# Performance work log

Hardware: AMD Instinct MI355X
Metric: run time of the kernel (lower is better)

The kernel has to match this reference:

```python
import jax, jax.numpy as jnp
import numpy as np

N = 50000


def gcn_conv(x, W, b, src, dst, deg_inv_sqrt):
    # h = x @ W, then symmetric-normalized aggregation with self-loops
    h = x @ W  # [N, out]
    norm = deg_inv_sqrt[src] * deg_inv_sqrt[dst]  # [E]
    agg = jax.ops.segment_sum(h[src] * norm[:, None], dst, num_segments=N)
    # self-loop contribution: norm_ii = deg_inv_sqrt[i]^2
    agg = agg + h * (deg_inv_sqrt * deg_inv_sqrt)[:, None]
    return agg + b


def setup_inputs() -> dict:
    key = jax.random.key(0)
    ks = jax.random.split(key, 8)
    F_in, H, C = 128, 128, 64
    x = jax.random.normal(ks[0], (N, F_in), dtype=jnp.float32)
    edge_index = jax.random.randint(ks[1], (2, 800000), 0, N, dtype=jnp.int64)
    s = 1.0 / np.sqrt(F_in)
    W1 = jax.random.uniform(ks[2], (F_in, H), jnp.float32, -s, s)
    b1 = jnp.zeros((H,), jnp.float32)
    W2 = jax.random.uniform(ks[3], (H, H), jnp.float32, -s, s)
    b2 = jnp.zeros((H,), jnp.float32)
    W3 = jax.random.uniform(ks[4], (H, C), jnp.float32, -s, s)
    b3 = jnp.zeros((C,), jnp.float32)
    return {"x": x, "edge_index": edge_index, "W1": W1, "b1": b1,
            "W2": W2, "b2": b2, "W3": W3, "b3": b3}


def reference(x, edge_index, W1, b1, W2, b2, W3, b3):
    src, dst = edge_index[0], edge_index[1]
    # degree with self-loops (edge weight 1): deg[i] = in-degree + 1
    deg = jnp.zeros((N,), x.dtype).at[dst].add(1.0) + 1.0
    dinv = jax.lax.rsqrt(deg)
    h = gcn_conv(x, W1, b1, src, dst, dinv)
    h = jax.nn.relu(h)  # dropout p=0 / eval -> identity
    h = gcn_conv(h, W2, b2, src, dst, dinv)
    h = jax.nn.relu(h)
    h = gcn_conv(h, W3, b3, src, dst, dinv)
    return jax.nn.log_softmax(h, axis=-1)
```

## Files before the change

### kernel.cpp

```cpp
#include <hip/hip_runtime.h>
#include <math.h>

typedef short short8 __attribute__((ext_vector_type(8)));
typedef float floatx4 __attribute__((ext_vector_type(4)));

#define CHUNK_SHIFT 13
#define NCHUNK 8

__device__ __forceinline__ float4 ld4(const float* p) { return *reinterpret_cast<const float4*>(p); }
__device__ __forceinline__ void st4(float* p, float4 v) { *reinterpret_cast<float4*>(p) = v; }

__device__ __forceinline__ float bf2f(unsigned int u) { return __uint_as_float(u << 16); }
__device__ __forceinline__ unsigned int f2bf1(float f) {
    unsigned int x = __float_as_uint(f);
    return (x + 0x7fffu + ((x >> 16) & 1u)) >> 16;
}
__device__ __forceinline__ unsigned int f2bf2(float lo, float hi) {
    return f2bf1(lo) | (f2bf1(hi) << 16);
}
__device__ __forceinline__ void unpack8(uint4 v, float* f) {
    f[0] = bf2f(v.x & 0xffffu); f[1] = bf2f(v.x >> 16);
    f[2] = bf2f(v.y & 0xffffu); f[3] = bf2f(v.y >> 16);
    f[4] = bf2f(v.z & 0xffffu); f[5] = bf2f(v.z >> 16);
    f[6] = bf2f(v.w & 0xffffu); f[7] = bf2f(v.w >> 16);
}

__device__ __forceinline__ int sum8(const int* __restrict__ p) {
    uint4 a = *reinterpret_cast<const uint4*>(p);
    uint4 b = *reinterpret_cast<const uint4*>(p + 4);
    return (int)(a.x + a.y + a.z + a.w + b.x + b.y + b.z + b.w);
}

__global__ __launch_bounds__(256) void k_count_prep(const int* __restrict__ src, const int* __restrict__ dst,
                                                    int* __restrict__ deg2, int* __restrict__ rank, int E, int nbE,
                                                    const float* __restrict__ W1, const float* __restrict__ W2,
                                                    const float* __restrict__ W3, unsigned short* __restrict__ Wt1,
                                                    unsigned short* __restrict__ Wt2, unsigned short* __restrict__ Wt3) {
    if ((int)blockIdx.x < nbE) {
        int e = blockIdx.x * 256 + threadIdx.x;
        if (e < E) {
            int c = src[e] >> CHUNK_SHIFT;
            rank[e] = atomicAdd(&deg2[dst[e] * NCHUNK + c], 1);
        }
    } else {
        int t = (blockIdx.x - nbE) * 256 + threadIdx.x;
        if (t < 16384) {
            int k = t & 127, n = t >> 7;
            Wt1[n * 128 + k] = (unsigned short)f2bf1(W1[(size_t)k * 128 + n]);
        } else if (t < 32768) {
            int u = t - 16384;
            int k = u & 127, n = u >> 7;
            Wt2[n * 128 + k] = (unsigned short)f2bf1(W2[(size_t)k * 128 + n]);
        } else if (t < 40960) {
            int u = t - 32768;
            int k = u & 127, n = u >> 7;
            Wt3[n * 128 + k] = (unsigned short)f2bf1(W3[(size_t)k * 64 + n]);
        }
    }
}

__global__ __launch_bounds__(256) void k_dinv_reduce(const int* __restrict__ deg2, float* __restrict__ dinv,
                                                     int* __restrict__ bsum, int n, int nbN) {
    __shared__ int s[256];
    int t = threadIdx.x;
    if ((int)blockIdx.x < nbN) {
        int i = blockIdx.x * 256 + t;
        if (i < n) {
            int d = sum8(deg2 + (size_t)i * NCHUNK);
            dinv[i] = 1.0f / sqrtf((float)d + 1.0f);
        }
        return;
    }
    int b = (int)blockIdx.x - nbN;
    int i = b * 256 + t;
    s[t] = (i < n) ? sum8(deg2 + (size_t)i * NCHUNK) : 0;
    __syncthreads();
    for (int off = 128; off > 0; off >>= 1) {
        if (t < off) s[t] += s[t + off];
        __syncthreads();
    }
    if (t == 0) bsum[b] = s[0];
}

__global__ __launch_bounds__(256) void k_scansmall_gemm1(const int* __restrict__ bsum, int* __restrict__ boff, int nb,
                                                         const float* __restrict__ X, const unsigned short* __restrict__ Wt,
                                                         const float* __restrict__ dinv,
                                                         unsigned short* __restrict__ O, int nrows) {
    constexpr int LDR = 136;
    __shared__ __align__(16) unsigned char smem[(64 * LDR + 128 * LDR) * 2];

    const int tid = threadIdx.x;
    if (blockIdx.x == 0) {
        int* s = (int*)smem;
        int v = (tid < nb) ? bsum[tid] : 0;
        s[tid] = v;
        __syncthreads();
        for (int off = 1; off < 256; off <<= 1) {
            int x = (tid >= off) ? s[tid - off] : 0;
            __syncthreads();
            s[tid] += x;
            __syncthreads();
        }
        if (tid < nb) boff[tid] = s[tid] - v;
        return;
    }

    unsigned short* sX = (unsigned short*)smem;
    unsigned short* sB = sX + 64 * LDR;
    const int row0 = ((int)blockIdx.x - 1) * 64;

#pragma unroll
    for (int i = 0; i < 4; ++i) {
        int idx = tid + i * 256;
        int r = idx >> 4, c8 = idx & 15;
        int grow = row0 + r;
        uint4 v = make_uint4(0, 0, 0, 0);
        if (grow < nrows) {
            float4 a = ld4(X + (size_t)grow * 128 + c8 * 8);
            float4 b = ld4(X + (size_t)grow * 128 + c8 * 8 + 4);
            v = make_uint4(f2bf2(a.x, a.y), f2bf2(a.z, a.w), f2bf2(b.x, b.y), f2bf2(b.z, b.w));
        }
        *reinterpret_cast<uint4*>(&sX[r * LDR + c8 * 8]) = v;
    }
#pragma unroll
    for (int i = 0; i < 8; ++i) {
        int idx = tid + i * 256;
        int nn = idx >> 4, c8 = idx & 15;
        *reinterpret_cast<uint4*>(&sB[nn * LDR + c8 * 8]) =
            *reinterpret_cast<const uint4*>(Wt + (size_t)nn * 128 + c8 * 8);
    }
    __syncthreads();

    const int lane = tid & 63;
    const int wave = tid >> 6;
    const int l15  = lane & 15;
    const int quad = lane >> 4;

    floatx4 acc[8];
#pragma unroll
    for (int j = 0; j < 8; ++j) acc[j] = (floatx4){0.f, 0.f, 0.f, 0.f};

    const unsigned short* xbase = &sX[(wave * 16 + l15) * LDR + quad * 8];
#pragma unroll
    for (int kk = 0; kk < 4; ++kk) {
        short8 xb = *reinterpret_cast<const short8*>(xbase + kk * 32);
#pragma unroll
        for (int j = 0; j < 8; ++j) {
            short8 wa = *reinterpret_cast<const short8*>(&sB[(j * 16 + l15) * LDR + quad * 8 + kk * 32]);
            acc[j] = __builtin_amdgcn_mfma_f32_16x16x32_bf16(wa, xb, acc[j], 0, 0, 0);
        }
    }

    int xrow = row0 + wave * 16 + l15;
    if (xrow < nrows) {
        float di = dinv[xrow];
#pragma unroll
        for (int j = 0; j < 8; ++j) {
            uint2 o = make_uint2(f2bf2(acc[j][0] * di, acc[j][1] * di), f2bf2(acc[j][2] * di, acc[j][3] * di));
            *reinterpret_cast<uint2*>(O + (size_t)xrow * 128 + j * 16 + quad * 4) = o;
        }
    }
}

__global__ __launch_bounds__(256) void k_scan_final(const int* __restrict__ deg2, const int* __restrict__ boff,
                                                    int* __restrict__ row_off, int* __restrict__ starts2,
                                                    int n) {
    __shared__ int s[256];
    int t = threadIdx.x;
    int i = blockIdx.x * 256 + t;
    uint4 d0 = make_uint4(0, 0, 0, 0), d1 = make_uint4(0, 0, 0, 0);
    int tot = 0;
    if (i < n) {
        d0 = *reinterpret_cast<const uint4*>(deg2 + (size_t)i * NCHUNK);
        d1 = *reinterpret_cast<const uint4*>(deg2 + (size_t)i * NCHUNK + 4);
        tot = (int)(d0.x + d0.y + d0.z + d0.w + d1.x + d1.y + d1.z + d1.w);
    }
    s[t] = tot;
    __syncthreads();
    for (int off = 1; off < 256; off <<= 1) {
        int x = (t >= off) ? s[t - off] : 0;
        __syncthreads();
        s[t] += x;
        __syncthreads();
    }
    int incl = s[t] + boff[blockIdx.x];
    if (i < n) {
        int r = incl - tot;
        row_off[i] = r;
        uint4 o0, o1;
        o0.x = r; r += d0.x;
        o0.y = r; r += d0.y;
        o0.z = r; r += d0.z;
        o0.w = r; r += d0.w;
        o1.x = r; r += d1.x;
        o1.y = r; r += d1.y;
        o1.z = r; r += d1.z;
        o1.w = r;
        *reinterpret_cast<uint4*>(starts2 + (size_t)i * NCHUNK) = o0;
        *reinterpret_cast<uint4*>(starts2 + (size_t)i * NCHUNK + 4) = o1;
        if (i == n - 1) row_off[n] = incl;
    }
}

__global__ __launch_bounds__(256) void k_fill(const int* __restrict__ src, const int* __restrict__ dst,
                                              const int* __restrict__ rank, const int* __restrict__ starts2,
                                              int* __restrict__ csrc, int E) {
    int e = blockIdx.x * 256 + threadIdx.x;
    if (e < E) {
        int s = src[e];
        int c = s >> CHUNK_SHIFT;
        csrc[starts2[dst[e] * NCHUNK + c] + rank[e]] = s;
    }
}

template <int NC>
__global__ __launch_bounds__(256) void k_gemm_mfma(const unsigned short* __restrict__ X,
                                                   const unsigned short* __restrict__ Wt,
                                                   const float* __restrict__ dinv,
                                                   unsigned short* __restrict__ O, int nrows) {
    constexpr int LDR = 136;
    __shared__ unsigned short sX[64 * LDR];
    __shared__ unsigned short sB[NC * LDR];

    const int tid  = threadIdx.x;
    const int row0 = blockIdx.x * 64;

#pragma unroll
    for (int i = 0; i < 4; ++i) {
        int idx = tid + i * 256;
        int r = idx >> 4, c8 = idx & 15;
        int grow = row0 + r;
        uint4 v = make_uint4(0, 0, 0, 0);
        if (grow < nrows) v = *reinterpret_cast<const uint4*>(X + (size_t)grow * 128 + c8 * 8);
        *reinterpret_cast<uint4*>(&sX[r * LDR + c8 * 8]) = v;
    }
#pragma unroll
    for (int i = 0; i < NC / 16; ++i) {
        int idx = tid + i * 256;
        int n = idx >> 4, c8 = idx & 15;
        *reinterpret_cast<uint4*>(&sB[n * LDR + c8 * 8]) =
            *reinterpret_cast<const uint4*>(Wt + (size_t)n * 128 + c8 * 8);
    }
    __syncthreads();

    const int lane = tid & 63;
    const int wave = tid >> 6;
    const int l15  = lane & 15;
    const int quad = lane >> 4;

    floatx4 acc[NC / 16];
#pragma unroll
    for (int j = 0; j < NC / 16; ++j) acc[j] = (floatx4){0.f, 0.f, 0.f, 0.f};

    const unsigned short* xbase = &sX[(wave * 16 + l15) * LDR + quad * 8];
#pragma unroll
    for (int kk = 0; kk < 4; ++kk) {
        short8 xb = *reinterpret_cast<const short8*>(xbase + kk * 32);
#pragma unroll
        for (int j = 0; j < NC / 16; ++j) {
            short8 wa = *reinterpret_cast<const short8*>(&sB[(j * 16 + l15) * LDR + quad * 8 + kk * 32]);
            acc[j] = __builtin_amdgcn_mfma_f32_16x16x32_bf16(wa, xb, acc[j], 0, 0, 0);
        }
    }

    int xrow = row0 + wave * 16 + l15;
    if (xrow < nrows) {
        float di = dinv[xrow];
#pragma unroll
        for (int j = 0; j < NC / 16; ++j) {
            uint2 o = make_uint2(f2bf2(acc[j][0] * di, acc[j][1] * di), f2bf2(acc[j][2] * di, acc[j][3] * di));
            *reinterpret_cast<uint2*>(O + (size_t)xrow * NC + j * 16 + quad * 4) = o;
        }
    }
}

__global__ __launch_bounds__(256) void k_agg_relu(const unsigned short* __restrict__ H, const int* __restrict__ roff,
                                                  const int* __restrict__ csrc, const float* __restrict__ dinv,
                                                  const float* __restrict__ bias, unsigned short* __restrict__ O, int n) {
    int t      = blockIdx.x * 256 + threadIdx.x;
    int node   = t >> 5;
    int lane32 = t & 31;
    int half   = lane32 >> 4;
    int f8     = (lane32 & 15) * 8;
    if (node >= n) return;

    float a[8];
    if (half == 0) {
        uint4 hv = *reinterpret_cast<const uint4*>(H + (size_t)node * 128 + f8);
        unpack8(hv, a);
    } else {
#pragma unroll
        for (int i = 0; i < 8; ++i) a[i] = 0.0f;
    }

    int e0 = roff[node];
    int e1 = roff[node + 1];
    int mid = e0 + ((e1 - e0) >> 1);
    int e  = half ? mid : e0;
    int ee = half ? e1 : mid;

    for (; e + 3 < ee; e += 4) {
        int s[4];
        uint4 v[4];
#pragma unroll
        for (int u = 0; u < 4; ++u) s[u] = csrc[e + u];
#pragma unroll
        for (int u = 0; u < 4; ++u) v[u] = *reinterpret_cast<const uint4*>(H + (size_t)s[u] * 128 + f8);
#pragma unroll
        for (int u = 0; u < 4; ++u) {
            float g2[8];
            unpack8(v[u], g2);
#pragma unroll
            for (int i = 0; i < 8; ++i) a[i] += g2[i];
        }
    }
    for (; e < ee; ++e) {
        uint4 v0 = *reinterpret_cast<const uint4*>(H + (size_t)csrc[e] * 128 + f8);
        float g0[8];
        unpack8(v0, g0);
#pragma unroll
        for (int i = 0; i < 8; ++i) a[i] += g0[i];
    }

#pragma unroll
    for (int i = 0; i < 8; ++i) a[i] += __shfl_xor(a[i], 16);

    if (half == 0) {
        float di = dinv[node];
        float4 b0 = ld4(bias + f8);
        float4 b1 = ld4(bias + f8 + 4);
        float bb[8] = {b0.x, b0.y, b0.z, b0.w, b1.x, b1.y, b1.z, b1.w};
#pragma unroll
        for (int i = 0; i < 8; ++i) a[i] = fmaxf(a[i] * di + bb[i], 0.0f);

        uint4 ov = make_uint4(f2bf2(a[0], a[1]), f2bf2(a[2], a[3]), f2bf2(a[4], a[5]), f2bf2(a[6], a[7]));
        *reinterpret_cast<uint4*>(O + (size_t)node * 128 + f8) = ov;
    }
}

__global__ __launch_bounds__(256) void k_agg_softmax(const unsigned short* __restrict__ H, const int* __restrict__ roff,
                                                     const int* __restrict__ csrc, const float* __restrict__ dinv,
                                                     const float* __restrict__ bias, float* __restrict__ O, int n) {
    int t      = blockIdx.x * 256 + threadIdx.x;
    int node   = t >> 4;
    int lane16 = t & 15;
    int half   = lane16 >> 3;
    int f8     = (lane16 & 7) * 8;
    if (node >= n) return;

    float a[8];
    if (half == 0) {
        uint4 hv = *reinterpret_cast<const uint4*>(H + (size_t)node * 64 + f8);
        unpack8(hv, a);
    } else {
#pragma unroll
        for (int i = 0; i < 8; ++i) a[i] = 0.0f;
    }

    int e0 = roff[node];
    int e1 = roff[node + 1];
    int mid = e0 + ((e1 - e0) >> 1);
    int e  = half ? mid : e0;
    int ee = half ? e1 : mid;

    for (; e + 3 < ee; e += 4) {
        int s[4];
        uint4 v[4];
#pragma unroll
        for (int u = 0; u < 4; ++u) s[u] = csrc[e + u];
#pragma unroll
        for (int u = 0; u < 4; ++u) v[u] = *reinterpret_cast<const uint4*>(H + (size_t)s[u] * 64 + f8);
#pragma unroll
        for (int u = 0; u < 4; ++u) {
            float gg[8];
            unpack8(v[u], gg);
#pragma unroll
            for (int i = 0; i < 8; ++i) a[i] += gg[i];
        }
    }
    for (; e < ee; ++e) {
        uint4 v0 = *reinterpret_cast<const uint4*>(H + (size_t)csrc[e] * 64 + f8);
        float g0[8];
        unpack8(v0, g0);
#pragma unroll
        for (int i = 0; i < 8; ++i) a[i] += g0[i];
    }

#pragma unroll
    for (int i = 0; i < 8; ++i) a[i] += __shfl_xor(a[i], 8);

    if (half == 0) {
        float di = dinv[node];
        float4 b0 = ld4(bias + f8);
        float4 b1 = ld4(bias + f8 + 4);
        float bb[8] = {b0.x, b0.y, b0.z, b0.w, b1.x, b1.y, b1.z, b1.w};
        float v[8];
#pragma unroll
        for (int i = 0; i < 8; ++i) v[i] = a[i] * di + bb[i];

        float m = v[0];
#pragma unroll
        for (int i = 1; i < 8; ++i) m = fmaxf(m, v[i]);
        m = fmaxf(m, __shfl_xor(m, 1));
        m = fmaxf(m, __shfl_xor(m, 2));
        m = fmaxf(m, __shfl_xor(m, 4));

        float ssum = 0.0f;
#pragma unroll
        for (int i = 0; i < 8; ++i) ssum += expf(v[i] - m);
        ssum += __shfl_xor(ssum, 1);
        ssum += __shfl_xor(ssum, 2);
        ssum += __shfl_xor(ssum, 4);
        float ls = logf(ssum);

        float* op = O + (size_t)node * 64 + f8;
        st4(op, make_float4(v[0] - m - ls, v[1] - m - ls, v[2] - m - ls, v[3] - m - ls));
        st4(op + 4, make_float4(v[4] - m - ls, v[5] - m - ls, v[6] - m - ls, v[7] - m - ls));
    }
}

extern "C" void kernel_launch(void* const* d_in, const int* in_sizes, int n_in,
                              void* d_out, int out_size, void* d_ws, size_t ws_size,
                              hipStream_t stream) {
    const float* x  = (const float*)d_in[0];
    const int*   ei = (const int*)d_in[1];
    const float* W1 = (const float*)d_in[2];
    const float* b1 = (const float*)d_in[3];
    const float* W2 = (const float*)d_in[4];
    const float* b2 = (const float*)d_in[5];
    const float* W3 = (const float*)d_in[6];
    const float* b3 = (const float*)d_in[7];
    float* out = (float*)d_out;

    const int N = in_sizes[0] / 128;
    const int E = in_sizes[1] / 2;
    const int* src = ei;
    const int* dst = ei + E;

    char* ws = (char*)d_ws;
    size_t off = 0;
    auto alloc = [&](size_t bytes) -> char* {
        char* p = ws + off;
        off = (off + bytes + 255) & ~(size_t)255;
        return p;
    };
    int nb  = (N + 255) / 256;
    int nbE = (E + 255) / 256;
    int blocks64 = (N + 63) / 64;

    int*   deg2    = (int*)alloc((size_t)N * NCHUNK * 4);
    int*   row_off = (int*)alloc(((size_t)N + 1) * 4);
    int*   starts2 = (int*)alloc((size_t)N * NCHUNK * 4);
    float* dinv    = (float*)alloc((size_t)N * 4);
    int*   bsum    = (int*)alloc((size_t)nb * 4);
    int*   boff    = (int*)alloc((size_t)nb * 4);
    int*   rank    = (int*)alloc((size_t)E * 4);
    int*   csrc    = (int*)alloc((size_t)E * 4);
    unsigned short* Wt1  = (unsigned short*)alloc(128 * 128 * 2);
    unsigned short* Wt2  = (unsigned short*)alloc(128 * 128 * 2);
    unsigned short* Wt3  = (unsigned short*)alloc(64 * 128 * 2);
    unsigned short* bufA = (unsigned short*)alloc((size_t)N * 128 * 2);
    unsigned short* bufB = (unsigned short*)alloc((size_t)N * 128 * 2);
    unsigned short* bufC = (unsigned short*)alloc((size_t)N * 64 * 2);
    (void)ws_size; (void)n_in; (void)out_size;

    hipMemsetAsync(deg2, 0, (size_t)N * NCHUNK * 4, stream);
    k_count_prep<<<nbE + 160, 256, 0, stream>>>(src, dst, deg2, rank, E, nbE, W1, W2, W3, Wt1, Wt2, Wt3);
    k_dinv_reduce<<<nb + nb, 256, 0, stream>>>(deg2, dinv, bsum, N, nb);
    k_scansmall_gemm1<<<1 + blocks64, 256, 0, stream>>>(bsum, boff, nb, x, Wt1, dinv, bufA, N);
    k_scan_final<<<nb, 256, 0, stream>>>(deg2, boff, row_off, starts2, N);
    k_fill<<<nbE, 256, 0, stream>>>(src, dst, rank, starts2, csrc, E);

    k_agg_relu<<<((size_t)N * 32 + 255) / 256, 256, 0, stream>>>(bufA, row_off, csrc, dinv, b1, bufB, N);
    k_gemm_mfma<128><<<blocks64, 256, 0, stream>>>(bufB, Wt2, dinv, bufA, N);
    k_agg_relu<<<((size_t)N * 32 + 255) / 256, 256, 0, stream>>>(bufA, row_off, csrc, dinv, b2, bufB, N);
    k_gemm_mfma<64><<<blocks64, 256, 0, stream>>>(bufB, Wt3, dinv, bufC, N);
    k_agg_softmax<<<((size_t)N * 16 + 255) / 256, 256, 0, stream>>>(bufC, row_off, csrc, dinv, b3, out, N);
}
```

Before: 252.1 us.

## Merge preprocessing and first GEMM into one cooperative kernel with grid syncs

Replaces the memset and five preprocessing launches (degree count, reduce, scan, fill, first GEMM) with a single cooperative kernel that steps through the phases using grid-wide syncs, with grid-stride loops for the edge and GEMM work. The aim is to remove launch and inter-kernel drain overhead between many small dependent stages. In exchange the grid is capped by occupancy (up to 2048 blocks), grid.sync has its own cost, and the GEMM tile loop now runs with fewer resident blocks. Correctness of the scan phases assumes the grid has at least nb blocks, which holds for 2048 blocks.

```diff
diff --git a/kernel.cpp b/kernel.cpp
--- a/kernel.cpp
+++ b/kernel.cpp
@@ -1,5 +1,8 @@
 #include <hip/hip_runtime.h>
+#include <hip/hip_cooperative_groups.h>
 #include <math.h>
+
+namespace cg = cooperative_groups;
 
 typedef short short8 __attribute__((ext_vector_type(8)));
 typedef float floatx4 __attribute__((ext_vector_type(4)));
@@ -31,185 +34,174 @@
     return (int)(a.x + a.y + a.z + a.w + b.x + b.y + b.z + b.w);
 }
 
-__global__ __launch_bounds__(256) void k_count_prep(const int* __restrict__ src, const int* __restrict__ dst,
-                                                    int* __restrict__ deg2, int* __restrict__ rank, int E, int nbE,
-                                                    const float* __restrict__ W1, const float* __restrict__ W2,
-                                                    const float* __restrict__ W3, unsigned short* __restrict__ Wt1,
-                                                    unsigned short* __restrict__ Wt2, unsigned short* __restrict__ Wt3) {
-    if ((int)blockIdx.x < nbE) {
-        int e = blockIdx.x * 256 + threadIdx.x;
-        if (e < E) {
-            int c = src[e] >> CHUNK_SHIFT;
-            rank[e] = atomicAdd(&deg2[dst[e] * NCHUNK + c], 1);
-        }
-    } else {
-        int t = (blockIdx.x - nbE) * 256 + threadIdx.x;
-        if (t < 16384) {
-            int k = t & 127, n = t >> 7;
-            Wt1[n * 128 + k] = (unsigned short)f2bf1(W1[(size_t)k * 128 + n]);
-        } else if (t < 32768) {
-            int u = t - 16384;
-            int k = u & 127, n = u >> 7;
-            Wt2[n * 128 + k] = (unsigned short)f2bf1(W2[(size_t)k * 128 + n]);
-        } else if (t < 40960) {
-            int u = t - 32768;
-            int k = u & 127, n = u >> 7;
-            Wt3[n * 128 + k] = (unsigned short)f2bf1(W3[(size_t)k * 64 + n]);
-        }
-    }
-}
-
-__global__ __launch_bounds__(256) void k_dinv_reduce(const int* __restrict__ deg2, float* __restrict__ dinv,
-                                                     int* __restrict__ bsum, int n, int nbN) {
-    __shared__ int s[256];
-    int t = threadIdx.x;
-    if ((int)blockIdx.x < nbN) {
-        int i = blockIdx.x * 256 + t;
-        if (i < n) {
-            int d = sum8(deg2 + (size_t)i * NCHUNK);
-            dinv[i] = 1.0f / sqrtf((float)d + 1.0f);
-        }
-        return;
-    }
-    int b = (int)blockIdx.x - nbN;
-    int i = b * 256 + t;
-    s[t] = (i < n) ? sum8(deg2 + (size_t)i * NCHUNK) : 0;
-    __syncthreads();
-    for (int off = 128; off > 0; off >>= 1) {
-        if (t < off) s[t] += s[t + off];
-        __syncthreads();
-    }
-    if (t == 0) bsum[b] = s[0];
-}
-
-__global__ __launch_bounds__(256) void k_scansmall_gemm1(const int* __restrict__ bsum, int* __restrict__ boff, int nb,
-                                                         const float* __restrict__ X, const unsigned short* __restrict__ Wt,
-                                                         const float* __restrict__ dinv,
-                                                         unsigned short* __restrict__ O, int nrows) {
+__global__ __launch_bounds__(256) void k_prep_all(
+    const int* __restrict__ src, const int* __restrict__ dst,
+    int* __restrict__ deg2, int* __restrict__ rank,
+    int* __restrict__ bsum, int* __restrict__ boff,
+    int* __restrict__ row_off, int* __restrict__ starts2,
+    float* __restrict__ dinv, int* __restrict__ csrc,
+    const float* __restrict__ X, const float* __restrict__ W1,
+    const float* __restrict__ W2, const float* __restrict__ W3,
+    unsigned short* __restrict__ Wt1, unsigned short* __restrict__ Wt2,
+    unsigned short* __restrict__ Wt3, unsigned short* __restrict__ O1,
+    int n, int E, int nb, int tiles) {
+    cg::grid_group grid = cg::this_grid();
     constexpr int LDR = 136;
     __shared__ __align__(16) unsigned char smem[(64 * LDR + 128 * LDR) * 2];
+    int* sInt = (int*)smem;
 
     const int tid = threadIdx.x;
-    if (blockIdx.x == 0) {
-        int* s = (int*)smem;
+    const int bid = (int)blockIdx.x;
+    const int gt  = bid * 256 + tid;
+    const int gs  = (int)gridDim.x * 256;
+
+    for (int i = gt; i < n * NCHUNK; i += gs) deg2[i] = 0;
+    for (int t = gt; t < 40960; t += gs) {
+        if (t < 16384) {
+            int k = t & 127, nn = t >> 7;
+            Wt1[nn * 128 + k] = (unsigned short)f2bf1(W1[(size_t)k * 128 + nn]);
+        } else if (t < 32768) {
+            int u = t - 16384, k = u & 127, nn = u >> 7;
+            Wt2[nn * 128 + k] = (unsigned short)f2bf1(W2[(size_t)k * 128 + nn]);
+        } else {
+            int u = t - 32768, k = u & 127, nn = u >> 7;
+            Wt3[nn * 128 + k] = (unsigned short)f2bf1(W3[(size_t)k * 64 + nn]);
+        }
+    }
+    grid.sync();
+
+    for (int e = gt; e < E; e += gs) {
+        int c = src[e] >> CHUNK_SHIFT;
+        rank[e] = atomicAdd(&deg2[dst[e] * NCHUNK + c], 1);
+    }
+    grid.sync();
+
+    if (bid < nb) {
+        int i = bid * 256 + tid;
+        sInt[tid] = (i < n) ? sum8(deg2 + (size_t)i * NCHUNK) : 0;
+        __syncthreads();
+        for (int off = 128; off > 0; off >>= 1) {
+            if (tid < off) sInt[tid] += sInt[tid + off];
+            __syncthreads();
+        }
+        if (tid == 0) bsum[bid] = sInt[0];
+    }
+    grid.sync();
+
+    if (bid == 0) {
         int v = (tid < nb) ? bsum[tid] : 0;
-        s[tid] = v;
+        sInt[tid] = v;
         __syncthreads();
         for (int off = 1; off < 256; off <<= 1) {
-            int x = (tid >= off) ? s[tid - off] : 0;
+            int x = (tid >= off) ? sInt[tid - off] : 0;
             __syncthreads();
-            s[tid] += x;
+            sInt[tid] += x;
             __syncthreads();
         }
-        if (tid < nb) boff[tid] = s[tid] - v;
-        return;
+        if (tid < nb) boff[tid] = sInt[tid] - v;
+    }
+    grid.sync();
+
+    if (bid < nb) {
+        int i = bid * 256 + tid;
+        uint4 d0 = make_uint4(0, 0, 0, 0), d1 = make_uint4(0, 0, 0, 0);
+        int tot = 0;
+        if (i < n) {
+            d0 = *reinterpret_cast<const uint4*>(deg2 + (size_t)i * NCHUNK);
+            d1 = *reinterpret_cast<const uint4*>(deg2 + (size_t)i * NCHUNK + 4);
+            tot = (int)(d0.x + d0.y + d0.z + d0.w + d1.x + d1.y + d1.z + d1.w);
+        }
+        sInt[tid] = tot;
+        __syncthreads();
+        for (int off = 1; off < 256; off <<= 1) {
+            int x = (tid >= off) ? sInt[tid - off] : 0;
+            __syncthreads();
+            sInt[tid] += x;
+            __syncthreads();
+        }
+        int incl = sInt[tid] + boff[bid];
+        if (i < n) {
+            int r = incl - tot;
+            row_off[i] = r;
+            uint4 o0, o1;
+            o0.x = r; r += d0.x;
+            o0.y = r; r += d0.y;
+            o0.z = r; r += d0.z;
+            o0.w = r; r += d0.w;
+            o1.x = r; r += d1.x;
+            o1.y = r; r += d1.y;
+            o1.z = r; r += d1.z;
+            o1.w = r;
+            *reinterpret_cast<uint4*>(starts2 + (size_t)i * NCHUNK) = o0;
+            *reinterpret_cast<uint4*>(starts2 + (size_t)i * NCHUNK + 4) = o1;
+            dinv[i] = 1.0f / sqrtf((float)tot + 1.0f);
+            if (i == n - 1) row_off[n] = incl;
+        }
+    }
+    grid.sync();
+
+    for (int e = gt; e < E; e += gs) {
+        int s = src[e];
+        int c = s >> CHUNK_SHIFT;
+        csrc[starts2[dst[e] * NCHUNK + c] + rank[e]] = s;
     }
 
     unsigned short* sX = (unsigned short*)smem;
     unsigned short* sB = sX + 64 * LDR;
-    const int row0 = ((int)blockIdx.x - 1) * 64;
-
-#pragma unroll
-    for (int i = 0; i < 4; ++i) {
-        int idx = tid + i * 256;
-        int r = idx >> 4, c8 = idx & 15;
-        int grow = row0 + r;
-        uint4 v = make_uint4(0, 0, 0, 0);
-        if (grow < nrows) {
-            float4 a = ld4(X + (size_t)grow * 128 + c8 * 8);
-            float4 b = ld4(X + (size_t)grow * 128 + c8 * 8 + 4);
-            v = make_uint4(f2bf2(a.x, a.y), f2bf2(a.z, a.w), f2bf2(b.x, b.y), f2bf2(b.z, b.w));
-        }
-        *reinterpret_cast<uint4*>(&sX[r * LDR + c8 * 8]) = v;
-    }
-#pragma unroll
-    for (int i = 0; i < 8; ++i) {
-        int idx = tid + i * 256;
-        int nn = idx >> 4, c8 = idx & 15;
-        *reinterpret_cast<uint4*>(&sB[nn * LDR + c8 * 8]) =
-            *reinterpret_cast<const uint4*>(Wt + (size_t)nn * 128 + c8 * 8);
-    }
-    __syncthreads();
-
     const int lane = tid & 63;
     const int wave = tid >> 6;
     const int l15  = lane & 15;
     const int quad = lane >> 4;
 
-    floatx4 acc[8];
-#pragma unroll
-    for (int j = 0; j < 8; ++j) acc[j] = (floatx4){0.f, 0.f, 0.f, 0.f};
-
-    const unsigned short* xbase = &sX[(wave * 16 + l15) * LDR + quad * 8];
-#pragma unroll
-    for (int kk = 0; kk < 4; ++kk) {
-        short8 xb = *reinterpret_cast<const short8*>(xbase + kk * 32);
-#pragma unroll
-        for (int j = 0; j < 8; ++j) {
-            short8 wa = *reinterpret_cast<const short8*>(&sB[(j * 16 + l15) * LDR + quad * 8 + kk * 32]);
-            acc[j] = __builtin_amdgcn_mfma_f32_16x16x32_bf16(wa, xb, acc[j], 0, 0, 0);
-        }
-    }
-
-    int xrow = row0 + wave * 16 + l15;
-    if (xrow < nrows) {
-        float di = dinv[xrow];
-#pragma unroll
-        for (int j = 0; j < 8; ++j) {
-            uint2 o = make_uint2(f2bf2(acc[j][0] * di, acc[j][1] * di), f2bf2(acc[j][2] * di, acc[j][3] * di));
-            *reinterpret_cast<uint2*>(O + (size_t)xrow * 128 + j * 16 + quad * 4) = o;
-        }
-    }
-}
-
-__global__ __launch_bounds__(256) void k_scan_final(const int* __restrict__ deg2, const int* __restrict__ boff,
-                                                    int* __restrict__ row_off, int* __restrict__ starts2,
-                                                    int n) {
-    __shared__ int s[256];
-    int t = threadIdx.x;
-    int i = blockIdx.x * 256 + t;
-    uint4 d0 = make_uint4(0, 0, 0, 0), d1 = make_uint4(0, 0, 0, 0);
-    int tot = 0;
-    if (i < n) {
-        d0 = *reinterpret_cast<const uint4*>(deg2 + (size_t)i * NCHUNK);
-        d1 = *reinterpret_cast<const uint4*>(deg2 + (size_t)i * NCHUNK + 4);
-        tot = (int)(d0.x + d0.y + d0.z + d0.w + d1.x + d1.y + d1.z + d1.w);
-    }
-    s[t] = tot;
-    __syncthreads();
-    for (int off = 1; off < 256; off <<= 1) {
-        int x = (t >= off) ? s[t - off] : 0;
+    for (int tile = bid; tile < tiles; tile += (int)gridDim.x) {
         __syncthreads();
-        s[t] += x;
+        const int row0 = tile * 64;
+#pragma unroll
+        for (int i = 0; i < 4; ++i) {
+            int idx = tid + i * 256;
+            int r = idx >> 4, c8 = idx & 15;
+            int grow = row0 + r;
+            uint4 v = make_uint4(0, 0, 0, 0);
+            if (grow < n) {
+                float4 a = ld4(X + (size_t)grow * 128 + c8 * 8);
+                float4 b = ld4(X + (size_t)grow * 128 + c8 * 8 + 4);
+                v = make_uint4(f2bf2(a.x, a.y), f2bf2(a.z, a.w), f2bf2(b.x, b.y), f2bf2(b.z, b.w));
+            }
+            *reinterpret_cast<uint4*>(&sX[r * LDR + c8 * 8]) = v;
+        }
+#pragma unroll
+        for (int i = 0; i < 8; ++i) {
+            int idx = tid + i * 256;
+            int nn = idx >> 4, c8 = idx & 15;
+            *reinterpret_cast<uint4*>(&sB[nn * LDR + c8 * 8]) =
+                *reinterpret_cast<const uint4*>(Wt1 + (size_t)nn * 128 + c8 * 8);
+        }
         __syncthreads();
-    }
-    int incl = s[t] + boff[blockIdx.x];
-    if (i < n) {
-        int r = incl - tot;
-        row_off[i] = r;
-        uint4 o0, o1;
-        o0.x = r; r += d0.x;
-        o0.y = r; r += d0.y;
-        o0.z = r; r += d0.z;
-        o0.w = r; r += d0.w;
-        o1.x = r; r += d1.x;
-        o1.y = r; r += d1.y;
-        o1.z = r; r += d1.z;
-        o1.w = r;
-        *reinterpret_cast<uint4*>(starts2 + (size_t)i * NCHUNK) = o0;
-        *reinterpret_cast<uint4*>(starts2 + (size_t)i * NCHUNK + 4) = o1;
-        if (i == n - 1) row_off[n] = incl;
-    }
-}
-
-__global__ __launch_bounds__(256) void k_fill(const int* __restrict__ src, const int* __restrict__ dst,
-                                              const int* __restrict__ rank, const int* __restrict__ starts2,
-                                              int* __restrict__ csrc, int E) {
-    int e = blockIdx.x * 256 + threadIdx.x;
-    if (e < E) {
-        int s = src[e];
-        int c = s >> CHUNK_SHIFT;
-        csrc[starts2[dst[e] * NCHUNK + c] + rank[e]] = s;
+
+        floatx4 acc[8];
+#pragma unroll
+        for (int j = 0; j < 8; ++j) acc[j] = (floatx4){0.f, 0.f, 0.f, 0.f};
+
+        const unsigned short* xbase = &sX[(wave * 16 + l15) * LDR + quad * 8];
+#pragma unroll
+        for (int kk = 0; kk < 4; ++kk) {
+            short8 xb = *reinterpret_cast<const short8*>(xbase + kk * 32);
+#pragma unroll
+            for (int j = 0; j < 8; ++j) {
+                short8 wa = *reinterpret_cast<const short8*>(&sB[(j * 16 + l15) * LDR + quad * 8 + kk * 32]);
+                acc[j] = __builtin_amdgcn_mfma_f32_16x16x32_bf16(wa, xb, acc[j], 0, 0, 0);
+            }
+        }
+
+        int xrow = row0 + wave * 16 + l15;
+        if (xrow < n) {
+            float di = dinv[xrow];
+#pragma unroll
+            for (int j = 0; j < 8; ++j) {
+                uint2 o = make_uint2(f2bf2(acc[j][0] * di, acc[j][1] * di), f2bf2(acc[j][2] * di, acc[j][3] * di));
+                *reinterpret_cast<uint2*>(O1 + (size_t)xrow * 128 + j * 16 + quad * 4) = o;
+            }
+        }
     }
 }
 
@@ -445,7 +437,6 @@
         return p;
     };
     int nb  = (N + 255) / 256;
-    int nbE = (E + 255) / 256;
     int blocks64 = (N + 63) / 64;
 
     int*   deg2    = (int*)alloc((size_t)N * NCHUNK * 4);
@@ -464,12 +455,24 @@
     unsigned short* bufC = (unsigned short*)alloc((size_t)N * 64 * 2);
     (void)ws_size; (void)n_in; (void)out_size;
 
-    hipMemsetAsync(deg2, 0, (size_t)N * NCHUNK * 4, stream);
-    k_count_prep<<<nbE + 160, 256, 0, stream>>>(src, dst, deg2, rank, E, nbE, W1, W2, W3, Wt1, Wt2, Wt3);
-    k_dinv_reduce<<<nb + nb, 256, 0, stream>>>(deg2, dinv, bsum, N, nb);
-    k_scansmall_gemm1<<<1 + blocks64, 256, 0, stream>>>(bsum, boff, nb, x, Wt1, dinv, bufA, N);
-    k_scan_final<<<nb, 256, 0, stream>>>(deg2, boff, row_off, starts2, N);
-    k_fill<<<nbE, 256, 0, stream>>>(src, dst, rank, starts2, csrc, E);
+    static int coopBlocks = 0;
+    if (coopBlocks == 0) {
+        int mb = 0;
+        if (hipOccupancyMaxActiveBlocksPerMultiprocessor(&mb, k_prep_all, 256, 0) != hipSuccess || mb <= 0)
+            mb = 2;
+        coopBlocks = mb * 256;
+        if (coopBlocks > 2048) coopBlocks = 2048;
+    }
+
+    int N_ = N, E_ = E, nb_ = nb, tiles_ = blocks64;
+    void* kargs[] = {
+        (void*)&src, (void*)&dst, (void*)&deg2, (void*)&rank,
+        (void*)&bsum, (void*)&boff, (void*)&row_off, (void*)&starts2,
+        (void*)&dinv, (void*)&csrc,
+        (void*)&x, (void*)&W1, (void*)&W2, (void*)&W3,
+        (void*)&Wt1, (void*)&Wt2, (void*)&Wt3, (void*)&bufA,
+        (void*)&N_, (void*)&E_, (void*)&nb_, (void*)&tiles_};
+    hipLaunchCooperativeKernel((void*)k_prep_all, dim3(coopBlocks), dim3(256), kargs, 0, stream);
 
     k_agg_relu<<<((size_t)N * 32 + 255) / 256, 256, 0, stream>>>(bufA, row_off, csrc, dinv, b1, bufB, N);
     k_gemm_mfma<128><<<blocks64, 256, 0, stream>>>(bufB, Wt2, dinv, bufA, N);
```

Measured after the change: 529.3 us. 2.1x slower.
